# Kernel optimization log

Hardware: AMD Instinct MI355X
Metric: run time of the kernel (lower is better)

## Reference

```python
import jax, jax.numpy as jnp
import numpy as np

NEG_SLOPE = 0.1

def leaky(x):
    return jnp.where(x >= 0, x, NEG_SLOPE * x)

def setup_inputs() -> dict:
    key = jax.random.key(0)
    ks = jax.random.split(key, 8)
    B, N, K, C, CO = 8, 16384, 9, 64, 64
    xy_offset = jax.random.normal(ks[0], (B, 2, N, K), dtype=jnp.float32)
    knn_features = jax.random.normal(ks[1], (B, C, N, K), dtype=jnp.float32)
    # WeightNet(2, [9, 9]): two 1x1 conv layers 2->9->9, leaky_relu after each
    wn_w1 = jax.random.normal(ks[2], (9, 2), dtype=jnp.float32) * (1.0 / np.sqrt(2))
    wn_b1 = jnp.zeros((9,), dtype=jnp.float32)
    wn_w2 = jax.random.normal(ks[3], (9, 9), dtype=jnp.float32) * (1.0 / 3.0)
    wn_b2 = jnp.zeros((9,), dtype=jnp.float32)
    # Linear(9*(C+2) -> CO)
    fan_in = 9 * (C + 2)
    lin_w = jax.random.normal(ks[4], (CO, fan_in), dtype=jnp.float32) * (1.0 / np.sqrt(fan_in))
    lin_b = jnp.zeros((CO,), dtype=jnp.float32)
    return {"xy_offset": xy_offset, "knn_features": knn_features,
            "wn_w1": wn_w1, "wn_b1": wn_b1, "wn_w2": wn_w2, "wn_b2": wn_b2,
            "lin_w": lin_w, "lin_b": lin_b}

def reference(xy_offset, knn_features, wn_w1, wn_b1, wn_w2, wn_b2, lin_w, lin_b):
    B, _, N, K = xy_offset.shape
    # concat positional offsets with features: [B, C+2, N, K]
    knn = jnp.concatenate([xy_offset, knn_features], axis=1)
    knn_cl = knn.transpose(0, 2, 3, 1)                       # [B, N, K, C+2]
    # WeightNet: 1x1 convs over channel dim of xy_offset
    h = leaky(jnp.einsum('oc,bcnk->bonk', wn_w1, xy_offset) + wn_b1[None, :, None, None])
    w = leaky(jnp.einsum('oc,bcnk->bonk', wn_w2, h) + wn_b2[None, :, None, None])  # [B, 9, N, K]
    w = w.transpose(0, 2, 1, 3)                              # [B, N, 9, K]
    # per-point small matmul: [B, N, 9, K] @ [B, N, K, C+2] -> [B, N, 9, C+2]
    wf = jnp.einsum('bnok,bnkc->bnoc', w, knn_cl)
    wf = wf.reshape(B, N, -1)                                # [B, N, 9*(C+2)]
    wf = wf @ lin_w.T + lin_b                                # [B, N, CO]
    out = leaky(wf.transpose(0, 2, 1))                       # [B, CO, N], norm=Identity
    return out
```

## Files before the change

kernel.cpp:

```cpp
#include <hip/hip_runtime.h>
#include <hip/hip_bf16.h>

#define NB   8
#define NN   16384
#define NK   9
#define NCF  64
#define NCIN 66
#define NCO  64
#define JTOT (NCIN * NK)
#define KPAD 608
#define ROWE 610
#define ROWU (ROWE / 2)
#define MT   32
#define CHC  8
#define NCHUNK (NCF / CHC)
#define ROWB (MT * NK * 4)
#define TRC  (CHC * ROWB / 16)
#define INSC (TRC / 64)

typedef __attribute__((ext_vector_type(8))) short frag8;
typedef __attribute__((ext_vector_type(4))) float frag4;

__device__ __forceinline__ float leakyf(float x) { return fmaxf(x, 0.1f * x); }

__device__ __forceinline__ unsigned short f2bf(float x) {
  __hip_bfloat16 h = __float2bfloat16(x);
  unsigned short us;
  __builtin_memcpy(&us, &h, 2);
  return us;
}

__global__ void prep_lb_kernel(const float* __restrict__ lin_w, unsigned short* __restrict__ lb) {
  int idx = blockIdx.x * 256 + threadIdx.x;
  if (idx >= NCO * KPAD) return;
  int co = idx / KPAD;
  int j  = idx - co * KPAD;
  float v = 0.f;
  if (j < JTOT) {
    int c = j / NK;
    int o = j - c * NK;
    v = lin_w[co * JTOT + o * NCIN + c];
  }
  lb[idx] = f2bf(v);
}

__global__ __launch_bounds__(256) void pointconv_kernel(
    const float* __restrict__ xy,
    const float* __restrict__ feat,
    const float* __restrict__ w1,
    const float* __restrict__ b1,
    const float* __restrict__ w2,
    const float* __restrict__ b2,
    const unsigned short* __restrict__ lb,
    const float* __restrict__ lin_b,
    float* __restrict__ out) {
  __shared__ unsigned short wfs[MT * ROWE];
  __shared__ float stage[2][CHC * MT * NK];

  const int t    = threadIdx.x;
  const int p    = t & 31;
  const int g    = t >> 5;
  const int lane = t & 63;
  const int wvid = t >> 6;
  const int b    = blockIdx.x >> 9;
  const int n0   = (blockIdx.x & 511) << 5;
  const int n    = n0 + p;

  auto stage_chunk = [&](int ch, float* dst) {
    const char* gb = (const char*)feat +
        (((size_t)b * NCF + ch * CHC) * NN + (size_t)n0) * (NK * 4);
    for (int i = wvid; i < INSC; i += 4) {
      unsigned j   = i * 64 + lane;
      unsigned cl  = j / 72u;
      unsigned rem = j - cl * 72u;
      const char* gp = gb + (size_t)cl * ((size_t)NN * NK * 4) + rem * 16;
      const char* lp = (const char*)dst + i * 1024;
      __builtin_amdgcn_global_load_lds(
          (const __attribute__((address_space(1))) unsigned int*)gp,
          (__attribute__((address_space(3))) unsigned int*)lp,
          16, 0, 0);
    }
  };

  stage_chunk(0, stage[0]);

  float wv[9][9];
  float x0[9], x1[9];
  {
    const float* x0p = xy + (((size_t)b * 2 + 0) * NN + n) * NK;
    const float* x1p = xy + (((size_t)b * 2 + 1) * NN + n) * NK;
#pragma unroll
    for (int k = 0; k < NK; ++k) { x0[k] = x0p[k]; x1[k] = x1p[k]; }
#pragma unroll
    for (int k = 0; k < NK; ++k) {
      float h[9];
#pragma unroll
      for (int o = 0; o < 9; ++o)
        h[o] = leakyf(w1[2 * o] * x0[k] + w1[2 * o + 1] * x1[k] + b1[o]);
#pragma unroll
      for (int o = 0; o < 9; ++o) {
        float s = b2[o];
#pragma unroll
        for (int o2 = 0; o2 < 9; ++o2) s += w2[o * 9 + o2] * h[o2];
        wv[o][k] = leakyf(s);
      }
    }
  }

  if (g == 0) {
#pragma unroll
    for (int cc = 0; cc < 2; ++cc) {
#pragma unroll
      for (int o = 0; o < 9; ++o) {
        float s = wv[o][0] * (cc ? x1[0] : x0[0]);
#pragma unroll
        for (int k = 1; k < NK; ++k) s += wv[o][k] * (cc ? x1[k] : x0[k]);
        wfs[p * ROWE + cc * 9 + o] = f2bf(s);
      }
    }
  }
  if (g == 1) {
#pragma unroll
    for (int m = 0; m < KPAD - JTOT; ++m) wfs[p * ROWE + JTOT + m] = 0;
  }

  for (int ch = 0; ch < NCHUNK; ++ch) {
    __syncthreads();
    if (ch + 1 < NCHUNK) stage_chunk(ch + 1, stage[(ch + 1) & 1]);
    {
      const float* sp = stage[ch & 1] + g * (MT * NK) + p * NK;
      float f[9];
#pragma unroll
      for (int k = 0; k < NK; ++k) f[k] = sp[k];
      const int c = 2 + ch * CHC + g;
      unsigned short* wr = wfs + p * ROWE + c * 9;
#pragma unroll
      for (int o = 0; o < 9; ++o) {
        float s = wv[o][0] * f[0];
#pragma unroll
        for (int k = 1; k < NK; ++k) s += wv[o][k] * f[k];
        wr[o] = f2bf(s);
      }
    }
  }
  __syncthreads();

  const unsigned int* wfu = (const unsigned int*)wfs;
  const int r    = wvid & 1;
  const int hh   = wvid >> 1;
  const int col  = lane & 15;
  const int q    = lane >> 4;

  frag4 acc[2];
#pragma unroll
  for (int ct = 0; ct < 2; ++ct) acc[ct] = frag4{0.f, 0.f, 0.f, 0.f};

  const int arow_u = (16 * r + col) * ROWU;

  for (int s = 0; s < KPAD / 32; ++s) {
    const int k0 = 32 * s;
    union { unsigned int u[4]; frag8 v; } ua;
    const int abase = arow_u + ((k0 + q * 8) >> 1);
    ua.u[0] = wfu[abase + 0];
    ua.u[1] = wfu[abase + 1];
    ua.u[2] = wfu[abase + 2];
    ua.u[3] = wfu[abase + 3];
#pragma unroll
    for (int ct = 0; ct < 2; ++ct) {
      const frag8* bp = (const frag8*)(lb + ((2 * hh + ct) * 16 + col) * KPAD + k0 + q * 8);
      acc[ct] = __builtin_amdgcn_mfma_f32_16x16x32_bf16(ua.v, *bp, acc[ct], 0, 0, 0);
    }
  }

  float* outbase = out + ((size_t)b * NCO) * NN;
  const int nrow = n0 + 16 * r + q * 4;
#pragma unroll
  for (int ct = 0; ct < 2; ++ct) {
    const int co = (2 * hh + ct) * 16 + col;
    const float bias = lin_b[co];
    float4 v;
    v.x = leakyf(acc[ct][0] + bias);
    v.y = leakyf(acc[ct][1] + bias);
    v.z = leakyf(acc[ct][2] + bias);
    v.w = leakyf(acc[ct][3] + bias);
    *(float4*)(outbase + (size_t)co * NN + nrow) = v;
  }
}

extern "C" void kernel_launch(void* const* d_in, const int* in_sizes, int n_in,
                              void* d_out, int out_size, void* d_ws, size_t ws_size,
                              hipStream_t stream) {
  const float* xy    = (const float*)d_in[0];
  const float* feat  = (const float*)d_in[1];
  const float* w1    = (const float*)d_in[2];
  const float* b1    = (const float*)d_in[3];
  const float* w2    = (const float*)d_in[4];
  const float* b2    = (const float*)d_in[5];
  const float* lw    = (const float*)d_in[6];
  const float* lbias = (const float*)d_in[7];
  float* out = (float*)d_out;
  unsigned short* lb = (unsigned short*)d_ws;

  prep_lb_kernel<<<(NCO * KPAD + 255) / 256, 256, 0, stream>>>(lw, lb);
  pointconv_kernel<<<NB * (NN / MT), 256, 0, stream>>>(
      xy, feat, w1, b1, w2, b2, lb, lbias, out);
}
```

Before: 471.7 us.

## Triple-buffer feature staging with smaller chunks and vmcnt-based waits

Feature staging now uses three LDS buffers of 4 channels instead of two of 8, keeping two chunks in flight. The full __syncthreads is replaced by explicit s_waitcnt vmcnt plus s_barrier, and the first two prefetches are issued before the WeightNet compute. The aim is to hide global-load latency better, and the smaller staging buffers cut LDS use, which may allow more resident blocks. The cost is twice as many loop iterations and barriers, and groups g and g+4 now compute the same channel redundantly.

Result: slower. 508.5 us (+7.8%).

```diff
diff --git a/kernel.cpp b/kernel.cpp
--- a/kernel.cpp
+++ b/kernel.cpp
@@ -12,11 +12,11 @@
 #define ROWE 610
 #define ROWU (ROWE / 2)
 #define MT   32
-#define CHC  8
+#define CHC  4
 #define NCHUNK (NCF / CHC)
+#define NSTG 3
 #define ROWB (MT * NK * 4)
 #define TRC  (CHC * ROWB / 16)
-#define INSC (TRC / 64)
 
 typedef __attribute__((ext_vector_type(8))) short frag8;
 typedef __attribute__((ext_vector_type(4))) float frag4;
@@ -55,7 +55,7 @@
     const float* __restrict__ lin_b,
     float* __restrict__ out) {
   __shared__ unsigned short wfs[MT * ROWE];
-  __shared__ float stage[2][CHC * MT * NK];
+  __shared__ float stage[NSTG][CHC * MT * NK];
 
   const int t    = threadIdx.x;
   const int p    = t & 31;
@@ -69,41 +69,54 @@
   auto stage_chunk = [&](int ch, float* dst) {
     const char* gb = (const char*)feat +
         (((size_t)b * NCF + ch * CHC) * NN + (size_t)n0) * (NK * 4);
-    for (int i = wvid; i < INSC; i += 4) {
-      unsigned j   = i * 64 + lane;
+    {
+      unsigned j   = wvid * 64u + lane;
       unsigned cl  = j / 72u;
       unsigned rem = j - cl * 72u;
       const char* gp = gb + (size_t)cl * ((size_t)NN * NK * 4) + rem * 16;
-      const char* lp = (const char*)dst + i * 1024;
+      const char* lp = (const char*)dst + wvid * 1024;
       __builtin_amdgcn_global_load_lds(
           (const __attribute__((address_space(1))) unsigned int*)gp,
           (__attribute__((address_space(3))) unsigned int*)lp,
           16, 0, 0);
     }
+    if (wvid == 0 && lane < 32) {
+      unsigned j   = 256u + lane;
+      unsigned cl  = j / 72u;
+      unsigned rem = j - cl * 72u;
+      const char* gp = gb + (size_t)cl * ((size_t)NN * NK * 4) + rem * 16;
+      const char* lp = (const char*)dst + 4096;
+      __builtin_amdgcn_global_load_lds(
+          (const __attribute__((address_space(1))) unsigned int*)gp,
+          (__attribute__((address_space(3))) unsigned int*)lp,
+          16, 0, 0);
+    }
   };
 
-  stage_chunk(0, stage[0]);
-
-  float wv[9][9];
   float x0[9], x1[9];
   {
     const float* x0p = xy + (((size_t)b * 2 + 0) * NN + n) * NK;
     const float* x1p = xy + (((size_t)b * 2 + 1) * NN + n) * NK;
 #pragma unroll
     for (int k = 0; k < NK; ++k) { x0[k] = x0p[k]; x1[k] = x1p[k]; }
-#pragma unroll
-    for (int k = 0; k < NK; ++k) {
-      float h[9];
-#pragma unroll
-      for (int o = 0; o < 9; ++o)
-        h[o] = leakyf(w1[2 * o] * x0[k] + w1[2 * o + 1] * x1[k] + b1[o]);
-#pragma unroll
-      for (int o = 0; o < 9; ++o) {
-        float s = b2[o];
-#pragma unroll
-        for (int o2 = 0; o2 < 9; ++o2) s += w2[o * 9 + o2] * h[o2];
-        wv[o][k] = leakyf(s);
-      }
+  }
+
+  stage_chunk(0, stage[0]);
+  stage_chunk(1, stage[1]);
+
+  float wv[9][9];
+#pragma unroll
+  for (int k = 0; k < NK; ++k) {
+    float h[9];
+#pragma unroll
+    for (int o = 0; o < 9; ++o)
+      h[o] = leakyf(w1[2 * o] * x0[k] + w1[2 * o + 1] * x1[k] + b1[o]);
+#pragma unroll
+    for (int o = 0; o < 9; ++o) {
+      float s = b2[o];
+#pragma unroll
+      for (int o2 = 0; o2 < 9; ++o2) s += w2[o * 9 + o2] * h[o2];
+      wv[o][k] = leakyf(s);
     }
   }
 
@@ -124,15 +137,27 @@
     for (int m = 0; m < KPAD - JTOT; ++m) wfs[p * ROWE + JTOT + m] = 0;
   }
 
+  int bcur = 0;
   for (int ch = 0; ch < NCHUNK; ++ch) {
-    __syncthreads();
-    if (ch + 1 < NCHUNK) stage_chunk(ch + 1, stage[(ch + 1) & 1]);
+    if (ch == NCHUNK - 1) {
+      asm volatile("s_waitcnt vmcnt(0)" ::: "memory");
+    } else if (wvid == 0) {
+      asm volatile("s_waitcnt vmcnt(2)" ::: "memory");
+    } else {
+      asm volatile("s_waitcnt vmcnt(1)" ::: "memory");
+    }
+    __builtin_amdgcn_s_barrier();
+
+    if (ch + 2 < NCHUNK) {
+      int bnxt = bcur + 2; if (bnxt >= NSTG) bnxt -= NSTG;
+      stage_chunk(ch + 2, stage[bnxt]);
+    }
     {
-      const float* sp = stage[ch & 1] + g * (MT * NK) + p * NK;
+      const float* sp = stage[bcur] + (g & 3) * (MT * NK) + p * NK;
       float f[9];
 #pragma unroll
       for (int k = 0; k < NK; ++k) f[k] = sp[k];
-      const int c = 2 + ch * CHC + g;
+      const int c = 2 + ch * CHC + (g & 3);
       unsigned short* wr = wfs + p * ROWE + c * 9;
 #pragma unroll
       for (int o = 0; o < 9; ++o) {
@@ -142,6 +167,7 @@
         wr[o] = f2bf(s);
       }
     }
+    bcur = (bcur == NSTG - 1) ? 0 : bcur + 1;
   }
   __syncthreads();
 
```

## Replace LDS double-buffered feature staging with direct per-thread global loads

Applied to the files above, without the earlier changes.

Removes the async global-to-LDS double-buffered staging of knn_features and the per-chunk barriers. Each thread now loads its own 9 contiguous floats per channel straight from global memory in a fully unrolled loop over 8 channels. This cuts LDS usage and synchronisation, which may allow more resident blocks, but gives up the coalesced 16-byte bulk transfers and the overlap of loads with compute. Per-thread strided 36-byte scalar loads may coalesce less efficiently.

Measured after the change: 465.4 us. About the same (-1.3%).

```diff
diff --git a/kernel.cpp b/kernel.cpp
--- a/kernel.cpp
+++ b/kernel.cpp
@@ -12,11 +12,6 @@
 #define ROWE 610
 #define ROWU (ROWE / 2)
 #define MT   32
-#define CHC  8
-#define NCHUNK (NCF / CHC)
-#define ROWB (MT * NK * 4)
-#define TRC  (CHC * ROWB / 16)
-#define INSC (TRC / 64)
 
 typedef __attribute__((ext_vector_type(8))) short frag8;
 typedef __attribute__((ext_vector_type(4))) float frag4;
@@ -55,7 +50,6 @@
     const float* __restrict__ lin_b,
     float* __restrict__ out) {
   __shared__ unsigned short wfs[MT * ROWE];
-  __shared__ float stage[2][CHC * MT * NK];
 
   const int t    = threadIdx.x;
   const int p    = t & 31;
@@ -66,44 +60,27 @@
   const int n0   = (blockIdx.x & 511) << 5;
   const int n    = n0 + p;
 
-  auto stage_chunk = [&](int ch, float* dst) {
-    const char* gb = (const char*)feat +
-        (((size_t)b * NCF + ch * CHC) * NN + (size_t)n0) * (NK * 4);
-    for (int i = wvid; i < INSC; i += 4) {
-      unsigned j   = i * 64 + lane;
-      unsigned cl  = j / 72u;
-      unsigned rem = j - cl * 72u;
-      const char* gp = gb + (size_t)cl * ((size_t)NN * NK * 4) + rem * 16;
-      const char* lp = (const char*)dst + i * 1024;
-      __builtin_amdgcn_global_load_lds(
-          (const __attribute__((address_space(1))) unsigned int*)gp,
-          (__attribute__((address_space(3))) unsigned int*)lp,
-          16, 0, 0);
-    }
-  };
-
-  stage_chunk(0, stage[0]);
-
-  float wv[9][9];
   float x0[9], x1[9];
   {
     const float* x0p = xy + (((size_t)b * 2 + 0) * NN + n) * NK;
     const float* x1p = xy + (((size_t)b * 2 + 1) * NN + n) * NK;
 #pragma unroll
     for (int k = 0; k < NK; ++k) { x0[k] = x0p[k]; x1[k] = x1p[k]; }
+  }
+
+  float wv[9][9];
 #pragma unroll
-    for (int k = 0; k < NK; ++k) {
-      float h[9];
+  for (int k = 0; k < NK; ++k) {
+    float h[9];
 #pragma unroll
-      for (int o = 0; o < 9; ++o)
-        h[o] = leakyf(w1[2 * o] * x0[k] + w1[2 * o + 1] * x1[k] + b1[o]);
+    for (int o = 0; o < 9; ++o)
+      h[o] = leakyf(w1[2 * o] * x0[k] + w1[2 * o + 1] * x1[k] + b1[o]);
 #pragma unroll
-      for (int o = 0; o < 9; ++o) {
-        float s = b2[o];
+    for (int o = 0; o < 9; ++o) {
+      float s = b2[o];
 #pragma unroll
-        for (int o2 = 0; o2 < 9; ++o2) s += w2[o * 9 + o2] * h[o2];
-        wv[o][k] = leakyf(s);
-      }
+      for (int o2 = 0; o2 < 9; ++o2) s += w2[o * 9 + o2] * h[o2];
+      wv[o][k] = leakyf(s);
     }
   }
 
@@ -124,15 +101,15 @@
     for (int m = 0; m < KPAD - JTOT; ++m) wfs[p * ROWE + JTOT + m] = 0;
   }
 
-  for (int ch = 0; ch < NCHUNK; ++ch) {
-    __syncthreads();
-    if (ch + 1 < NCHUNK) stage_chunk(ch + 1, stage[(ch + 1) & 1]);
-    {
-      const float* sp = stage[ch & 1] + g * (MT * NK) + p * NK;
+  {
+    const float* fbase = feat + (((size_t)b * NCF + g) * NN + (size_t)n) * NK;
+#pragma unroll
+    for (int cc = 0; cc < 8; ++cc) {
+      const float* fp = fbase + (size_t)(cc * 8) * ((size_t)NN * NK);
       float f[9];
 #pragma unroll
-      for (int k = 0; k < NK; ++k) f[k] = sp[k];
-      const int c = 2 + ch * CHC + g;
+      for (int k = 0; k < NK; ++k) f[k] = fp[k];
+      const int c = 2 + cc * 8 + g;
       unsigned short* wr = wfs + p * ROWE + c * 9;
 #pragma unroll
       for (int o = 0; o < 9; ++o) {
@@ -143,6 +120,7 @@
       }
     }
   }
+
   __syncthreads();
 
   const unsigned int* wfu = (const unsigned int*)wfs;
```
